# Kernel optimization log

Measured on AMD Instinct MI355X. Metric: run time of the kernel, lower is better.

The kernel has to match this reference:

```python
import jax, jax.numpy as jnp
import numpy as np

NEGINF = -1e20

def setup_inputs() -> dict:
    key = jax.random.key(0)
    ks = jax.random.split(key, 8)
    N, K, T, H = 32, 32, 128, 768
    return {
        "contexts_encoded_1": jax.random.normal(ks[0], (N, 3, H), jnp.float32),
        "tracked_knowledge_use": jax.random.normal(ks[1], (N, H), jnp.float32),
        "pool_encoded_0": jax.random.normal(ks[2], (N, K, T, H), jnp.float32),
        "pool_encoded_1": jax.random.normal(ks[3], (N, K, H), jnp.float32),
        "pool_mask": jnp.ones((N, K, T), jnp.bool_),
        "ck_mask": jnp.ones((N, K), jnp.bool_),
        "label": jax.random.randint(ks[4], (N,), 0, K, jnp.int32),
        "pool_tokens": jax.random.randint(ks[5], (N, K, T), 0, 32000, jnp.int32),
        "W_cqk": jax.random.normal(ks[6], (H, 2 * H), jnp.float32) * 0.02,
        "b_cqk": jnp.zeros((H,), jnp.float32),
        "W_k": jax.random.normal(ks[7], (H, H), jnp.float32) * 0.02,
        "b_k": jnp.zeros((H,), jnp.float32),
    }

def reference(contexts_encoded_1, tracked_knowledge_use, pool_encoded_0, pool_encoded_1,
              pool_mask, ck_mask, label, pool_tokens, W_cqk, b_cqk, W_k, b_k):
    N, K, T, H = pool_encoded_0.shape
    query_use = contexts_encoded_1[:, 2, :]                      # [N,H]
    cqk = jnp.concatenate([query_use, tracked_knowledge_use], axis=1)  # [N,2H]
    cqk_pro = cqk @ W_cqk.T + b_cqk                              # [N,H]
    pool_use_pro = jnp.einsum('nkh,gh->nkg', pool_encoded_1, W_k) + b_k  # [N,K,H]
    score = jnp.einsum('nkh,nh->nk', pool_use_pro, cqk_pro)      # [N,K]
    score = jnp.where(ck_mask, score, NEGINF)
    ids = label                                                   # train mode
    b = jnp.arange(N)
    shifted_use = pool_encoded_1[b, ids]        # [N,H]
    shifted_encoded = pool_encoded_0[b, ids]    # [N,T,H]
    shifted_mask = pool_mask[b, ids]            # [N,T]
    shifted_index = pool_tokens[b, ids]         # [N,T]
    return (score, shifted_encoded, shifted_mask, shifted_use, shifted_index)
```

## Files before the change

kernel.cpp:

```cpp
#include <hip/hip_runtime.h>


#define NN 32
#define KK 32
#define TT 128
#define HH 768
#define HH2 1536
#define NEGINF_F (-1e20f)

#define OUT_SCORE 0
#define OUT_ENC   1024
#define OUT_MASK  3146752
#define OUT_USE   3150848
#define OUT_IDX   3175424

#define GW_ENC 786432
#define GW_USE 792576
#define GW_MSK 796672
#define GW_TOT 800768

__global__ __launch_bounds__(256) void k1_v_gather(
    const float* __restrict__ ce1,
    const float* __restrict__ tku,
    const float* __restrict__ pe0,
    const float* __restrict__ pe1,
    const int* __restrict__ pmask,
    const int* __restrict__ label,
    const int* __restrict__ ptok,
    const float* __restrict__ Wcqk,
    const float* __restrict__ bcqk,
    float* __restrict__ v,
    float* __restrict__ out)
{
    int b = blockIdx.x;
    if (b < 48) {
        int t = b * 256 + threadIdx.x;
        int pair = t / HH;
        int g = t - pair * HH;
        int n0 = pair, n1 = pair + 16;
        const float4* wr = (const float4*)(Wcqk + (size_t)g * HH2);
        const float4* q0 = (const float4*)(ce1 + ((size_t)n0 * 3 + 2) * HH);
        const float4* q1 = (const float4*)(ce1 + ((size_t)n1 * 3 + 2) * HH);
        const float4* u0 = (const float4*)(tku + (size_t)n0 * HH);
        const float4* u1 = (const float4*)(tku + (size_t)n1 * HH);
        float a0 = 0.f, a1 = 0.f;
#pragma unroll 4
        for (int j = 0; j < 192; ++j) {
            float4 w4 = wr[j];
            float4 x0 = q0[j];
            float4 x1 = q1[j];
            a0 += w4.x * x0.x + w4.y * x0.y + w4.z * x0.z + w4.w * x0.w;
            a1 += w4.x * x1.x + w4.y * x1.y + w4.z * x1.z + w4.w * x1.w;
        }
#pragma unroll 4
        for (int j = 0; j < 192; ++j) {
            float4 w4 = wr[192 + j];
            float4 x0 = u0[j];
            float4 x1 = u1[j];
            a0 += w4.x * x0.x + w4.y * x0.y + w4.z * x0.z + w4.w * x0.w;
            a1 += w4.x * x1.x + w4.y * x1.y + w4.z * x1.z + w4.w * x1.w;
        }
        float bb = bcqk[g];
        v[n0 * HH + g] = a0 + bb;
        v[n1 * HH + g] = a1 + bb;
    } else {
        int wid = (b - 48) * 256 + threadIdx.x;
        if (wid < GW_ENC) {
            int n = wid / 24576;
            int r = wid - n * 24576;
            int id = label[n];
            float4 val = ((const float4*)pe0)[(size_t)(n * KK + id) * 24576 + r];
            ((float4*)(out + OUT_ENC))[wid] = val;
        } else if (wid < GW_USE) {
            int e = wid - GW_ENC;
            int n = e / 192;
            int r = e - n * 192;
            int id = label[n];
            float4 val = ((const float4*)pe1)[(size_t)(n * KK + id) * 192 + r];
            ((float4*)(out + OUT_USE))[e] = val;
        } else if (wid < GW_MSK) {
            int e = wid - GW_USE;
            int n = e / TT;
            int t = e - n * TT;
            int id = label[n];
            out[OUT_MASK + e] = pmask[(size_t)(n * KK + id) * TT + t] ? 1.0f : 0.0f;
        } else {
            int e = wid - GW_MSK;
            int n = e / TT;
            int t = e - n * TT;
            int id = label[n];
            out[OUT_IDX + e] = (float)ptok[(size_t)(n * KK + id) * TT + t];
        }
    }
}

__global__ __launch_bounds__(256) void k2_w(
    const float* __restrict__ Wk,
    const float* __restrict__ v,
    float* __restrict__ w)
{
    int t = blockIdx.x * 256 + threadIdx.x;
    int pair = t / HH;
    int h = t - pair * HH;
    int n0 = pair, n1 = pair + 16;
    const float4* v0 = (const float4*)(v + (size_t)n0 * HH);
    const float4* v1 = (const float4*)(v + (size_t)n1 * HH);
    float a0 = 0.f, a1 = 0.f;
    for (int g4 = 0; g4 < 192; ++g4) {
        float4 x0 = v0[g4];
        float4 x1 = v1[g4];
        int g = g4 * 4;
        float w0 = Wk[(size_t)(g + 0) * HH + h];
        float w1 = Wk[(size_t)(g + 1) * HH + h];
        float w2 = Wk[(size_t)(g + 2) * HH + h];
        float w3 = Wk[(size_t)(g + 3) * HH + h];
        a0 += x0.x * w0 + x0.y * w1 + x0.z * w2 + x0.w * w3;
        a1 += x1.x * w0 + x1.y * w1 + x1.z * w2 + x1.w * w3;
    }
    w[(size_t)n0 * HH + h] = a0;
    w[(size_t)n1 * HH + h] = a1;
}

__global__ __launch_bounds__(256) void k3_score(
    const float* __restrict__ pe1,
    const float* __restrict__ v,
    const float* __restrict__ w,
    const float* __restrict__ bk,
    const int* __restrict__ ckm,
    float* __restrict__ out)
{
    __shared__ float wl[HH];
    __shared__ float cpart[4];
    int n = blockIdx.x;
    int tid = threadIdx.x;
    int lane = tid & 63;
    int wv = tid >> 6;

    float p = 0.f;
#pragma unroll
    for (int i = 0; i < 3; ++i) {
        int g = tid + 256 * i;
        wl[g] = w[(size_t)n * HH + g];
        p += bk[g] * v[(size_t)n * HH + g];
    }
#pragma unroll
    for (int m = 1; m < 64; m <<= 1) p += __shfl_xor(p, m, 64);
    if (lane == 0) cpart[wv] = p;
    __syncthreads();
    float c = cpart[0] + cpart[1] + cpart[2] + cpart[3];

    for (int k = wv; k < KK; k += 4) {
        const float* row = pe1 + (size_t)(n * KK + k) * HH;
        float acc = 0.f;
#pragma unroll
        for (int i = 0; i < 12; ++i) {
            int h = lane + 64 * i;
            acc += row[h] * wl[h];
        }
#pragma unroll
        for (int m = 1; m < 64; m <<= 1) acc += __shfl_xor(acc, m, 64);
        if (lane == 0) {
            float s = acc + c;
            out[OUT_SCORE + n * KK + k] = ckm[n * KK + k] ? s : NEGINF_F;
        }
    }
}

extern "C" void kernel_launch(void* const* d_in, const int* in_sizes, int n_in,
                              void* d_out, int out_size, void* d_ws, size_t ws_size,
                              hipStream_t stream)
{
    const float* ce1  = (const float*)d_in[0];
    const float* tku  = (const float*)d_in[1];
    const float* pe0  = (const float*)d_in[2];
    const float* pe1  = (const float*)d_in[3];
    const int* pmask  = (const int*)d_in[4];
    const int* ckm    = (const int*)d_in[5];
    const int* label  = (const int*)d_in[6];
    const int* ptok   = (const int*)d_in[7];
    const float* Wcqk = (const float*)d_in[8];
    const float* bcqk = (const float*)d_in[9];
    const float* Wk   = (const float*)d_in[10];
    const float* bk   = (const float*)d_in[11];

    float* out = (float*)d_out;
    float* v = (float*)d_ws;
    float* w = v + NN * HH;

    k1_v_gather<<<48 + 3128, 256, 0, stream>>>(ce1, tku, pe0, pe1, pmask,
                                               label, ptok, Wcqk, bcqk, v, out);
    k2_w<<<48, 256, 0, stream>>>(Wk, v, w);
    k3_score<<<32, 256, 0, stream>>>(pe1, v, w, bk, ckm, out);
}
```

Baseline: 572.3 us.

## Parallelize cqk projection across wavefronts and split-K the Wk GEMV

The cqk projection in k1 moves from one thread per output (serial 1536-long dot product, strided row reads) to one wavefront per pair of output rows times 8 batch rows. Lanes read the weights coalesced and the partial sums are combined with a shuffle reduction, using 384 blocks instead of 48. k2 is split four ways along the reduction dimension, giving 192 blocks that write partial results, and k3 adds the four partials back together. The aim is to fill more compute units in the latency-bound small-GEMV phases, at the cost of extra workspace traffic and shuffle overhead.

Result: faster. 485.7 us (-15.1%).

```diff
diff --git a/kernel.cpp b/kernel.cpp
--- a/kernel.cpp
+++ b/kernel.cpp
@@ -18,6 +18,8 @@
 #define GW_USE 792576
 #define GW_MSK 796672
 #define GW_TOT 800768
+
+#define VBLK 384
 
 __global__ __launch_bounds__(256) void k1_v_gather(
     const float* __restrict__ ce1,
@@ -33,38 +35,62 @@
     float* __restrict__ out)
 {
     int b = blockIdx.x;
-    if (b < 48) {
-        int t = b * 256 + threadIdx.x;
-        int pair = t / HH;
-        int g = t - pair * HH;
-        int n0 = pair, n1 = pair + 16;
-        const float4* wr = (const float4*)(Wcqk + (size_t)g * HH2);
-        const float4* q0 = (const float4*)(ce1 + ((size_t)n0 * 3 + 2) * HH);
-        const float4* q1 = (const float4*)(ce1 + ((size_t)n1 * 3 + 2) * HH);
-        const float4* u0 = (const float4*)(tku + (size_t)n0 * HH);
-        const float4* u1 = (const float4*)(tku + (size_t)n1 * HH);
-        float a0 = 0.f, a1 = 0.f;
-#pragma unroll 4
-        for (int j = 0; j < 192; ++j) {
-            float4 w4 = wr[j];
-            float4 x0 = q0[j];
-            float4 x1 = q1[j];
-            a0 += w4.x * x0.x + w4.y * x0.y + w4.z * x0.z + w4.w * x0.w;
-            a1 += w4.x * x1.x + w4.y * x1.y + w4.z * x1.z + w4.w * x1.w;
-        }
-#pragma unroll 4
-        for (int j = 0; j < 192; ++j) {
-            float4 w4 = wr[192 + j];
-            float4 x0 = u0[j];
-            float4 x1 = u1[j];
-            a0 += w4.x * x0.x + w4.y * x0.y + w4.z * x0.z + w4.w * x0.w;
-            a1 += w4.x * x1.x + w4.y * x1.y + w4.z * x1.z + w4.w * x1.w;
-        }
-        float bb = bcqk[g];
-        v[n0 * HH + g] = a0 + bb;
-        v[n1 * HH + g] = a1 + bb;
+    if (b < VBLK) {
+        int wid  = (b << 2) + (threadIdx.x >> 6);
+        int lane = threadIdx.x & 63;
+        int gp = wid >> 2;
+        int nb = wid & 3;
+        int g0 = gp << 1, g1 = g0 + 1;
+        const float4* w0 = (const float4*)(Wcqk + (size_t)g0 * HH2);
+        const float4* w1 = (const float4*)(Wcqk + (size_t)g1 * HH2);
+        float a0[8], a1[8];
+#pragma unroll
+        for (int i = 0; i < 8; ++i) { a0[i] = 0.f; a1[i] = 0.f; }
+#pragma unroll
+        for (int s = 0; s < 3; ++s) {
+            int j = lane + (s << 6);
+            float4 wa = w0[j];
+            float4 wb = w1[j];
+#pragma unroll
+            for (int i = 0; i < 8; ++i) {
+                int n = (nb << 3) + i;
+                float4 x = ((const float4*)(ce1 + ((size_t)n * 3 + 2) * HH))[j];
+                a0[i] = fmaf(wa.w, x.w, fmaf(wa.z, x.z, fmaf(wa.y, x.y, fmaf(wa.x, x.x, a0[i]))));
+                a1[i] = fmaf(wb.w, x.w, fmaf(wb.z, x.z, fmaf(wb.y, x.y, fmaf(wb.x, x.x, a1[i]))));
+            }
+        }
+#pragma unroll
+        for (int s = 0; s < 3; ++s) {
+            int j = lane + (s << 6);
+            float4 wa = w0[192 + j];
+            float4 wb = w1[192 + j];
+#pragma unroll
+            for (int i = 0; i < 8; ++i) {
+                int n = (nb << 3) + i;
+                float4 x = ((const float4*)(tku + (size_t)n * HH))[j];
+                a0[i] = fmaf(wa.w, x.w, fmaf(wa.z, x.z, fmaf(wa.y, x.y, fmaf(wa.x, x.x, a0[i]))));
+                a1[i] = fmaf(wb.w, x.w, fmaf(wb.z, x.z, fmaf(wb.y, x.y, fmaf(wb.x, x.x, a1[i]))));
+            }
+        }
+#pragma unroll
+        for (int m = 1; m < 64; m <<= 1) {
+#pragma unroll
+            for (int i = 0; i < 8; ++i) {
+                a0[i] += __shfl_xor(a0[i], m, 64);
+                a1[i] += __shfl_xor(a1[i], m, 64);
+            }
+        }
+        if (lane == 0) {
+            float bb0 = bcqk[g0], bb1 = bcqk[g1];
+#pragma unroll
+            for (int i = 0; i < 8; ++i) {
+                int n = (nb << 3) + i;
+                v[n * HH + g0] = a0[i] + bb0;
+                v[n * HH + g1] = a1[i] + bb1;
+            }
+        }
     } else {
-        int wid = (b - 48) * 256 + threadIdx.x;
+        int wid = (b - VBLK) * 256 + threadIdx.x;
         if (wid < GW_ENC) {
             int n = wid / 24576;
             int r = wid - n * 24576;
@@ -97,34 +123,38 @@
 __global__ __launch_bounds__(256) void k2_w(
     const float* __restrict__ Wk,
     const float* __restrict__ v,
-    float* __restrict__ w)
-{
-    int t = blockIdx.x * 256 + threadIdx.x;
+    float* __restrict__ wpart)
+{
+    int b = blockIdx.x;
+    int gs = b & 3;
+    int t = (b >> 2) * 256 + threadIdx.x;
     int pair = t / HH;
     int h = t - pair * HH;
     int n0 = pair, n1 = pair + 16;
-    const float4* v0 = (const float4*)(v + (size_t)n0 * HH);
-    const float4* v1 = (const float4*)(v + (size_t)n1 * HH);
+    const float4* v0 = (const float4*)(v + (size_t)n0 * HH) + gs * 48;
+    const float4* v1 = (const float4*)(v + (size_t)n1 * HH) + gs * 48;
+    const float* wkb = Wk + (size_t)(gs * 192) * HH + h;
     float a0 = 0.f, a1 = 0.f;
-    for (int g4 = 0; g4 < 192; ++g4) {
+#pragma unroll 4
+    for (int g4 = 0; g4 < 48; ++g4) {
         float4 x0 = v0[g4];
         float4 x1 = v1[g4];
-        int g = g4 * 4;
-        float w0 = Wk[(size_t)(g + 0) * HH + h];
-        float w1 = Wk[(size_t)(g + 1) * HH + h];
-        float w2 = Wk[(size_t)(g + 2) * HH + h];
-        float w3 = Wk[(size_t)(g + 3) * HH + h];
-        a0 += x0.x * w0 + x0.y * w1 + x0.z * w2 + x0.w * w3;
-        a1 += x1.x * w0 + x1.y * w1 + x1.z * w2 + x1.w * w3;
-    }
-    w[(size_t)n0 * HH + h] = a0;
-    w[(size_t)n1 * HH + h] = a1;
+        const float* wp = wkb + (size_t)(g4 * 4) * HH;
+        float w0 = wp[0];
+        float w1 = wp[HH];
+        float w2 = wp[2 * HH];
+        float w3 = wp[3 * HH];
+        a0 = fmaf(x0.w, w3, fmaf(x0.z, w2, fmaf(x0.y, w1, fmaf(x0.x, w0, a0))));
+        a1 = fmaf(x1.w, w3, fmaf(x1.z, w2, fmaf(x1.y, w1, fmaf(x1.x, w0, a1))));
+    }
+    wpart[(size_t)(gs * NN + n0) * HH + h] = a0;
+    wpart[(size_t)(gs * NN + n1) * HH + h] = a1;
 }
 
 __global__ __launch_bounds__(256) void k3_score(
     const float* __restrict__ pe1,
     const float* __restrict__ v,
-    const float* __restrict__ w,
+    const float* __restrict__ wpart,
     const float* __restrict__ bk,
     const int* __restrict__ ckm,
     float* __restrict__ out)
@@ -140,8 +170,11 @@
 #pragma unroll
     for (int i = 0; i < 3; ++i) {
         int g = tid + 256 * i;
-        wl[g] = w[(size_t)n * HH + g];
-        p += bk[g] * v[(size_t)n * HH + g];
+        size_t off = (size_t)n * HH + g;
+        float s = wpart[off] + wpart[(size_t)NN * HH + off]
+                + wpart[(size_t)2 * NN * HH + off] + wpart[(size_t)3 * NN * HH + off];
+        wl[g] = s;
+        p += bk[g] * v[off];
     }
 #pragma unroll
     for (int m = 1; m < 64; m <<= 1) p += __shfl_xor(p, m, 64);
@@ -185,10 +218,10 @@
 
     float* out = (float*)d_out;
     float* v = (float*)d_ws;
-    float* w = v + NN * HH;
-
-    k1_v_gather<<<48 + 3128, 256, 0, stream>>>(ce1, tku, pe0, pe1, pmask,
-                                               label, ptok, Wcqk, bcqk, v, out);
-    k2_w<<<48, 256, 0, stream>>>(Wk, v, w);
-    k3_score<<<32, 256, 0, stream>>>(pe1, v, w, bk, ckm, out);
-}
+    float* wpart = v + NN * HH;
+
+    k1_v_gather<<<VBLK + 3128, 256, 0, stream>>>(ce1, tku, pe0, pe1, pmask,
+                                                 label, ptok, Wcqk, bcqk, v, out);
+    k2_w<<<192, 256, 0, stream>>>(Wk, v, wpart);
+    k3_score<<<32, 256, 0, stream>>>(pe1, v, wpart, bk, ckm, out);
+}
```
